# Optimization experiments

Hardware: AMD Instinct MI355X
Metric: run time of the kernel (lower is better)

## Reference

```python
import jax, jax.numpy as jnp
import numpy as np

EMBED_DIM = 1024
NUM_HEADS = 16
HEAD_DIM = EMBED_DIM // NUM_HEADS


def setup_inputs() -> dict:
    key = jax.random.key(0)
    ks = jax.random.split(key, 9)
    s = 1.0 / np.sqrt(EMBED_DIM)
    x = jax.random.normal(ks[0], (2, 2048, EMBED_DIM), dtype=jnp.float32)
    Wq = jax.random.uniform(ks[1], (EMBED_DIM, EMBED_DIM), jnp.float32, -s, s)
    bq = jax.random.uniform(ks[2], (EMBED_DIM,), jnp.float32, -s, s)
    Wk = jax.random.uniform(ks[3], (EMBED_DIM, EMBED_DIM), jnp.float32, -s, s)
    bk = jax.random.uniform(ks[4], (EMBED_DIM,), jnp.float32, -s, s)
    Wv = jax.random.uniform(ks[5], (EMBED_DIM, EMBED_DIM), jnp.float32, -s, s)
    bv = jax.random.uniform(ks[6], (EMBED_DIM,), jnp.float32, -s, s)
    Wo = jax.random.uniform(ks[7], (EMBED_DIM, EMBED_DIM), jnp.float32, -s, s)
    bo = jax.random.uniform(ks[8], (EMBED_DIM,), jnp.float32, -s, s)
    return {"x": x, "Wq": Wq, "bq": bq, "Wk": Wk, "bk": bk,
            "Wv": Wv, "bv": bv, "Wo": Wo, "bo": bo}


def reference(x, Wq, bq, Wk, bk, Wv, bv, Wo, bo):
    B, N, C = x.shape
    H, D = NUM_HEADS, HEAD_DIM
    # nn.Linear: y = x @ W.T + b; here W stored as [in, out] so y = x @ W + b
    def split_heads(y):
        return y.reshape(B, N, H, D).transpose(0, 2, 1, 3)  # [B,H,N,D]
    q = split_heads(x @ Wq + bq)
    k = split_heads(x @ Wk + bk)
    v = split_heads(x @ Wv + bv)
    scores = jnp.einsum('bhnd,bhmd->bhnm', q, k) / jnp.sqrt(jnp.float32(D)).astype(x.dtype)
    attn = jax.nn.softmax(scores, axis=-1)
    ctx = jnp.einsum('bhnm,bhmd->bhnd', attn, v)
    ctx = ctx.transpose(0, 2, 1, 3).reshape(B, N, C)
    return ctx @ Wo + bo
```

## Files before the change

### kernel.cpp

```cpp
#include <hip/hip_runtime.h>
#include <hip/hip_bf16.h>
#include <stdint.h>
#include <stddef.h>

using bf16 = __hip_bfloat16;
using bf16x8 = __attribute__((ext_vector_type(8))) short;
using f32x4  = __attribute__((ext_vector_type(4))) float;
using f32x16 = __attribute__((ext_vector_type(16))) float;
typedef unsigned int u32x2 __attribute__((ext_vector_type(2)));
typedef unsigned int u32x4 __attribute__((ext_vector_type(4)));

#define MFMA16(a, b, c) __builtin_amdgcn_mfma_f32_16x16x32_bf16((a), (b), (c), 0, 0, 0)
#define MFMA32(a, b, c) __builtin_amdgcn_mfma_f32_32x32x16_bf16((a), (b), (c), 0, 0, 0)

#define GLD16(g, l)                                                            \
  __builtin_amdgcn_global_load_lds(                                            \
      (const __attribute__((address_space(1))) void*)(g),                      \
      (__attribute__((address_space(3))) void*)(l), 16, 0, 0)

__device__ __forceinline__ float exp2_fast(float x) {
#if __has_builtin(__builtin_amdgcn_exp2f)
  return __builtin_amdgcn_exp2f(x);
#else
  return __expf(x * 0.69314718056f);
#endif
}

__device__ __forceinline__ unsigned int cvtpk_bf16(float lo, float hi) {
  unsigned int r;
  asm("v_cvt_pk_bf16_f32 %0, %1, %2" : "=v"(r) : "v"(lo), "v"(hi));
  return r;
}

__device__ __forceinline__ void permswap(unsigned int& a, unsigned int& b, int hi) {
#if __has_builtin(__builtin_amdgcn_permlane32_swap)
  u32x2 r = __builtin_amdgcn_permlane32_swap(a, b, false, false);
  a = r.x;
  b = r.y;
#else
  unsigned int sa = __shfl_xor((unsigned int)a, 32, 64);
  unsigned int sb = __shfl_xor((unsigned int)b, 32, 64);
  unsigned int an = hi ? sb : a;
  unsigned int bn = hi ? b : sa;
  a = an; b = bn;
#endif
}


__global__ void convert_x(const float* __restrict__ x, bf16* __restrict__ out) {
  const int i = blockIdx.x * 256 + threadIdx.x;
  const float4 v = ((const float4*)x)[i];
  __hip_bfloat162* o2 = (__hip_bfloat162*)(out + (size_t)i * 4);
  o2[0] = __float22bfloat162_rn(make_float2(v.x, v.y));
  o2[1] = __float22bfloat162_rn(make_float2(v.z, v.w));
}

__global__ void convert_w(const float* __restrict__ W0, const float* __restrict__ W1,
                          const float* __restrict__ W2, const float* __restrict__ W3,
                          bf16* __restrict__ Wt) {
  __shared__ float t[32][33];
  const int bx = blockIdx.x;
  const int mat = bx >> 10;
  const float* W = (mat == 0) ? W0 : (mat == 1) ? W1 : (mat == 2) ? W2 : W3;
  const int rem = bx & 1023;
  const int k0 = (rem >> 5) * 32, n0 = (rem & 31) * 32;
  const int c = threadIdx.x & 31, r0 = (threadIdx.x >> 5) * 4;
#pragma unroll
  for (int i = 0; i < 4; ++i) {
    const int r = r0 + i;
    t[r][c] = W[(size_t)(k0 + r) * 1024 + n0 + c];
  }
  __syncthreads();
  bf16* dst = Wt + (size_t)mat * 1024 * 1024;
#pragma unroll
  for (int i = 0; i < 4; ++i) {
    const int rn = r0 + i;
    dst[(size_t)(n0 + rn) * 1024 + k0 + c] = __float2bfloat16(t[c][rn]);
  }
}

__global__ void concat_bias(const float* __restrict__ bq, const float* __restrict__ bk,
                            const float* __restrict__ bv, const float* __restrict__ bo,
                            float* __restrict__ dst) {
  const int i = blockIdx.x * 256 + threadIdx.x;
  const float* src = (i < 1024) ? bq : (i < 2048) ? bk : (i < 3072) ? bv : bo;
  dst[i] = src[i & 1023];
}


template <int MODE>
__global__ __launch_bounds__(256)
void gemm_bt(const bf16* __restrict__ A, const bf16* __restrict__ Bt,
             const float* __restrict__ bias,
             bf16* __restrict__ Qb, bf16* __restrict__ Kb, bf16* __restrict__ Vt,
             float* __restrict__ Of, int K) {
  __shared__ bf16 As[128 * 32];
  __shared__ bf16 Bs[128 * 32];
  const int tid = threadIdx.x;
  const int lane = tid & 63, w = tid >> 6;
  const int wr = w >> 1, wc = w & 1;
  const int lrow = lane & 15, lgk = lane >> 4;
  const int bm = blockIdx.y * 128, bn = blockIdx.x * 128;
  f32x4 acc[4][4] = {};
  const bf16* Ab = A + (size_t)bm * K;
  const bf16* Bb = Bt + (size_t)bn * K;
  const int e0 = tid, e1 = 256 + tid;

  for (int k0 = 0; k0 < K; k0 += 32) {
    GLD16(Ab + (size_t)(e0 >> 2) * K + k0 + (e0 & 3) * 8, As + e0 * 8);
    GLD16(Ab + (size_t)(e1 >> 2) * K + k0 + (e1 & 3) * 8, As + e1 * 8);
    GLD16(Bb + (size_t)(e0 >> 2) * K + k0 + (e0 & 3) * 8, Bs + e0 * 8);
    GLD16(Bb + (size_t)(e1 >> 2) * K + k0 + (e1 & 3) * 8, Bs + e1 * 8);
    asm volatile("s_waitcnt vmcnt(0)" ::: "memory");
    __syncthreads();
    bf16x8 af[4], bfr[4];
#pragma unroll
    for (int m = 0; m < 4; ++m)
      af[m] = *(const bf16x8*)(As + (wr * 64 + m * 16 + lrow) * 32 + lgk * 8);
#pragma unroll
    for (int n = 0; n < 4; ++n)
      bfr[n] = *(const bf16x8*)(Bs + (wc * 64 + n * 16 + lrow) * 32 + lgk * 8);
#pragma unroll
    for (int m = 0; m < 4; ++m)
#pragma unroll
      for (int n = 0; n < 4; ++n)
        acc[m][n] = MFMA16(af[m], bfr[n], acc[m][n]);
    __syncthreads();
  }

#pragma unroll
  for (int m = 0; m < 4; ++m) {
#pragma unroll
    for (int n = 0; n < 4; ++n) {
      const int col = bn + wc * 64 + n * 16 + lrow;
      const float bv_ = bias[col];
      const int row0 = bm + wr * 64 + m * 16 + lgk * 4;
      if (MODE == 0) {
        const int which = col >> 10;
        const int hd = col & 1023;
        const int h = hd >> 6, d = hd & 63;
#pragma unroll
        for (int j = 0; j < 4; ++j) {
          const int row = row0 + j;
          const int b = row >> 11, t = row & 2047;
          const int bh = b * 16 + h;
          const float v = acc[m][n][j] + bv_;
          if (which == 0)
            Qb[((size_t)bh * 2048 + t) * 64 + d] =
                __float2bfloat16(v * 0.18033688f);
          else if (which == 1)
            Kb[((size_t)bh * 2048 + t) * 64 + d] = __float2bfloat16(v);
          else
            Vt[((size_t)bh * 64 + d) * 2048 + t] = __float2bfloat16(v);
        }
      } else {
#pragma unroll
        for (int j = 0; j < 4; ++j) {
          const int row = row0 + j;
          Of[(size_t)row * 1024 + col] = acc[m][n][j] + bv_;
        }
      }
    }
  }
}

__global__ __launch_bounds__(256)
void attn_kernel(const bf16* __restrict__ Q, const bf16* __restrict__ Kb,
                 const bf16* __restrict__ Vt, bf16* __restrict__ ctx) {
  __shared__ bf16 Kl[2][64 * 64];
  __shared__ bf16 Vl[2][64 * 64];

  const int tid = threadIdx.x, lane = tid & 63, w = tid >> 6;
  const int lo5 = lane & 31, hi = lane >> 5;

  const int bid = blockIdx.x;
  const int xcd = bid & 7, idx = bid >> 3;
  const int bh = (xcd << 2) | (idx >> 4);
  const int qt = idx & 15;
  const int q0 = qt * 128 + w * 32;

  const bf16* Qbh = Q + (size_t)bh * 2048 * 64;
  const bf16* Kbh = Kb + (size_t)bh * 2048 * 64;
  const bf16* Vbh = Vt + (size_t)bh * 64 * 2048;

  bf16x8 qf[4];
#pragma unroll
  for (int f = 0; f < 4; ++f)
    qf[f] = *(const bf16x8*)(Qbh + (size_t)(q0 + lo5) * 64 + f * 16 + hi * 8);

  f32x16 o0 = {}, o1 = {};
  float m2 = -1e30f;
  float lsum = 0.f;

  auto stage = [&](int buf, int kv) {
#pragma unroll
    for (int i = 0; i < 2; ++i) {
      const int c = (w * 2 + i) * 64 + lane;
      const int r = c >> 3, j = c & 7;
      const int js = (j ^ (r & 7)) * 8;
      GLD16(Kbh + (size_t)(kv + r) * 64 + js, &Kl[buf][c * 8]);
      GLD16(Vbh + (size_t)r * 2048 + kv + js, &Vl[buf][c * 8]);
    }
  };

  stage(0, 0);
  asm volatile("s_waitcnt vmcnt(0)" ::: "memory");
  __builtin_amdgcn_s_barrier();
  __builtin_amdgcn_sched_barrier(0);

  for (int t = 0; t < 32; ++t) {
    const int cur = t & 1;
    const int kv = t << 6;
    if (t < 31) {
      stage(cur ^ 1, kv + 64);
      asm volatile("s_waitcnt vmcnt(4)" ::: "memory");
    } else {
      asm volatile("s_waitcnt vmcnt(0)" ::: "memory");
    }
    __builtin_amdgcn_s_barrier();
    __builtin_amdgcn_sched_barrier(0);

    bf16x8 kf[8], vf[8];
#pragma unroll
    for (int kt = 0; kt < 2; ++kt)
#pragma unroll
      for (int f = 0; f < 4; ++f) {
        const int r = kt * 32 + lo5;
        kf[kt * 4 + f] =
            *(const bf16x8*)(&Kl[cur][(r * 8 + (((f << 1) + hi) ^ (r & 7))) * 8]);
      }
#pragma unroll
    for (int dt = 0; dt < 2; ++dt)
#pragma unroll
      for (int ks = 0; ks < 4; ++ks) {
        const int r = dt * 32 + lo5;
        vf[dt * 4 + ks] =
            *(const bf16x8*)(&Vl[cur][(r * 8 + (((ks << 1) + hi) ^ (r & 7))) * 8]);
      }
    asm volatile("s_waitcnt lgkmcnt(0)" ::: "memory");
    __builtin_amdgcn_s_barrier();
    __builtin_amdgcn_sched_barrier(0);

    f32x16 s0 = {}, s1 = {};
#pragma unroll
    for (int f = 0; f < 4; ++f) s0 = MFMA32(kf[f], qf[f], s0);
#pragma unroll
    for (int f = 0; f < 4; ++f) s1 = MFMA32(kf[4 + f], qf[f], s1);

    float p[32];
#pragma unroll
    for (int j = 0; j < 16; ++j) { p[j] = s0[j]; p[16 + j] = s1[j]; }
    float pm = p[0];
#pragma unroll
    for (int j = 1; j < 32; ++j) pm = fmaxf(pm, p[j]);
    if (!__all(pm <= m2 + 11.5416f)) {
      const float mx = fmaxf(pm, __shfl_xor(pm, 32, 64));
      const float mn = fmaxf(m2, mx);
      const float corr = exp2_fast(m2 - mn);
      m2 = mn;
      lsum *= corr;
#pragma unroll
      for (int j = 0; j < 16; ++j) { o0[j] *= corr; o1[j] *= corr; }
    }
    float rs = 0.f;
#pragma unroll
    for (int j = 0; j < 32; ++j) {
      p[j] = exp2_fast(p[j] - m2);
      rs += p[j];
    }
    lsum += rs;

    bf16x8 pa[4];
#pragma unroll
    for (int ks = 0; ks < 4; ++ks) {
      const int b0 = ks * 8;
      unsigned int a0 = cvtpk_bf16(p[b0 + 0], p[b0 + 1]);
      unsigned int c0 = cvtpk_bf16(p[b0 + 4], p[b0 + 5]);
      unsigned int a1 = cvtpk_bf16(p[b0 + 2], p[b0 + 3]);
      unsigned int c1 = cvtpk_bf16(p[b0 + 6], p[b0 + 7]);
      permswap(a0, c0, hi);
      permswap(a1, c1, hi);
      u32x4 tt;
      tt.x = a0; tt.y = a1; tt.z = c0; tt.w = c1;
      pa[ks] = __builtin_bit_cast(bf16x8, tt);
    }

#pragma unroll
    for (int ks = 0; ks < 4; ++ks) {
      o0 = MFMA32(vf[ks], pa[ks], o0);
      o1 = MFMA32(vf[4 + ks], pa[ks], o1);
    }
  }

  lsum += __shfl_xor(lsum, 32, 64);
  const float inv = 1.f / lsum;
  const int b = bh >> 4, h = bh & 15;
  bf16* crow = ctx + (size_t)(b * 2048 + q0 + lo5) * 1024 + h * 64;
#pragma unroll
  for (int g = 0; g < 4; ++g) {
    uint2 pk0, pk1;
    pk0.x = cvtpk_bf16(o0[4 * g + 0] * inv, o0[4 * g + 1] * inv);
    pk0.y = cvtpk_bf16(o0[4 * g + 2] * inv, o0[4 * g + 3] * inv);
    pk1.x = cvtpk_bf16(o1[4 * g + 0] * inv, o1[4 * g + 1] * inv);
    pk1.y = cvtpk_bf16(o1[4 * g + 2] * inv, o1[4 * g + 3] * inv);
    *(uint2*)(crow + 8 * g + 4 * hi) = pk0;
    *(uint2*)(crow + 32 + 8 * g + 4 * hi) = pk1;
  }
}


extern "C" void kernel_launch(void* const* d_in, const int* in_sizes, int n_in,
                              void* d_out, int out_size, void* d_ws, size_t ws_size,
                              hipStream_t stream) {
  const float* x  = (const float*)d_in[0];
  const float* Wq = (const float*)d_in[1];
  const float* bq = (const float*)d_in[2];
  const float* Wk = (const float*)d_in[3];
  const float* bk = (const float*)d_in[4];
  const float* Wv = (const float*)d_in[5];
  const float* bv = (const float*)d_in[6];
  const float* Wo = (const float*)d_in[7];
  const float* bo = (const float*)d_in[8];
  float* out = (float*)d_out;

  char* ws = (char*)d_ws;
  bf16* xb  = (bf16*)(ws);
  bf16* Wt  = (bf16*)(ws + ((size_t)8 << 20));
  bf16* Qb  = (bf16*)(ws + ((size_t)16 << 20));
  bf16* Kb  = (bf16*)(ws + ((size_t)24 << 20));
  bf16* Vt  = (bf16*)(ws + ((size_t)32 << 20));
  bf16* ctx = (bf16*)(ws + ((size_t)40 << 20));
  float* ba = (float*)(ws + ((size_t)48 << 20));

  convert_x<<<dim3(4096), dim3(256), 0, stream>>>(x, xb);
  convert_w<<<dim3(4096), dim3(256), 0, stream>>>(Wq, Wk, Wv, Wo, Wt);
  concat_bias<<<dim3(16), dim3(256), 0, stream>>>(bq, bk, bv, bo, ba);

  gemm_bt<0><<<dim3(24, 32), dim3(256), 0, stream>>>(xb, Wt, ba, Qb, Kb, Vt, nullptr, 1024);

  attn_kernel<<<dim3(512), dim3(256), 0, stream>>>(Qb, Kb, Vt, ctx);

  gemm_bt<1><<<dim3(8, 32), dim3(256), 0, stream>>>(
      ctx, Wt + (size_t)3072 * 1024, ba + 3072, nullptr, nullptr, nullptr, out, 1024);
}
```

Before: 144.2 us.

## Software-pipeline attention softmax with next QK MFMA and stage V-transpose writes

```diff
diff --git a/kernel.cpp b/kernel.cpp
--- a/kernel.cpp
+++ b/kernel.cpp
@@ -24,6 +24,10 @@
 #else
   return __expf(x * 0.69314718056f);
 #endif
+}
+
+__device__ __forceinline__ float fmax3(float a, float b, float c) {
+  return fmaxf(fmaxf(a, b), c);
 }
 
 __device__ __forceinline__ unsigned int cvtpk_bf16(float lo, float hi) {
@@ -128,43 +132,80 @@
     __syncthreads();
   }
 
-#pragma unroll
-  for (int m = 0; m < 4; ++m) {
-#pragma unroll
-    for (int n = 0; n < 4; ++n) {
-      const int col = bn + wc * 64 + n * 16 + lrow;
-      const float bv_ = bias[col];
-      const int row0 = bm + wr * 64 + m * 16 + lgk * 4;
-      if (MODE == 0) {
-        const int which = col >> 10;
-        const int hd = col & 1023;
-        const int h = hd >> 6, d = hd & 63;
-#pragma unroll
-        for (int j = 0; j < 4; ++j) {
-          const int row = row0 + j;
-          const int b = row >> 11, t = row & 2047;
-          const int bh = b * 16 + h;
-          const float v = acc[m][n][j] + bv_;
-          if (which == 0)
-            Qb[((size_t)bh * 2048 + t) * 64 + d] =
-                __float2bfloat16(v * 0.18033688f);
-          else if (which == 1)
-            Kb[((size_t)bh * 2048 + t) * 64 + d] = __float2bfloat16(v);
-          else
-            Vt[((size_t)bh * 64 + d) * 2048 + t] = __float2bfloat16(v);
+  if constexpr (MODE == 0) {
+    if (bn >= 2048) {
+      __shared__ bf16 vstage[64][130];
+      const int b = bm >> 11;
+      const int t0 = bm & 2047;
+      const int h0 = (bn - 2048) >> 6;
+#pragma unroll
+      for (int h2 = 0; h2 < 2; ++h2) {
+        if (wr == h2) {
+#pragma unroll
+          for (int m = 0; m < 4; ++m)
+#pragma unroll
+            for (int n = 0; n < 4; ++n) {
+              const int cl = wc * 64 + n * 16 + lrow;
+              const float bv_ = bias[bn + cl];
+#pragma unroll
+              for (int j = 0; j < 4; ++j)
+                vstage[m * 16 + lgk * 4 + j][cl] =
+                    __float2bfloat16(acc[m][n][j] + bv_);
+            }
         }
-      } else {
-#pragma unroll
-        for (int j = 0; j < 4; ++j) {
-          const int row = row0 + j;
-          Of[(size_t)row * 1024 + col] = acc[m][n][j] + bv_;
+        __syncthreads();
+#pragma unroll
+        for (int it = 0; it < 32; ++it) {
+          const int c = it * 4 + w;
+          const int hh = h0 + (c >> 6), d = c & 63;
+          Vt[((size_t)(b * 16 + hh) * 64 + d) * 2048 + t0 + h2 * 64 + lane] =
+              vstage[lane][c];
         }
-      }
-    }
-  }
-}
-
-__global__ __launch_bounds__(256)
+        __syncthreads();
+      }
+    } else {
+#pragma unroll
+      for (int m = 0; m < 4; ++m) {
+#pragma unroll
+        for (int n = 0; n < 4; ++n) {
+          const int col = bn + wc * 64 + n * 16 + lrow;
+          const float bv_ = bias[col];
+          const int row0 = bm + wr * 64 + m * 16 + lgk * 4;
+          const int which = col >> 10;
+          const int hd = col & 1023;
+          const int h = hd >> 6, d = hd & 63;
+#pragma unroll
+          for (int j = 0; j < 4; ++j) {
+            const int row = row0 + j;
+            const int b = row >> 11, t = row & 2047;
+            const int bh = b * 16 + h;
+            const float v = acc[m][n][j] + bv_;
+            if (which == 0)
+              Qb[((size_t)bh * 2048 + t) * 64 + d] =
+                  __float2bfloat16(v * 0.18033688f);
+            else
+              Kb[((size_t)bh * 2048 + t) * 64 + d] = __float2bfloat16(v);
+          }
+        }
+      }
+    }
+  } else {
+#pragma unroll
+    for (int m = 0; m < 4; ++m) {
+#pragma unroll
+      for (int n = 0; n < 4; ++n) {
+        const int col = bn + wc * 64 + n * 16 + lrow;
+        const float bv_ = bias[col];
+        const int row0 = bm + wr * 64 + m * 16 + lgk * 4;
+#pragma unroll
+        for (int j = 0; j < 4; ++j)
+          Of[(size_t)(row0 + j) * 1024 + col] = acc[m][n][j] + bv_;
+      }
+    }
+  }
+}
+
+__global__ __launch_bounds__(256, 2)
 void attn_kernel(const bf16* __restrict__ Q, const bf16* __restrict__ Kb,
                  const bf16* __restrict__ Vt, bf16* __restrict__ ctx) {
   __shared__ bf16 Kl[2][64 * 64];
@@ -203,56 +244,23 @@
     }
   };
 
-  stage(0, 0);
-  asm volatile("s_waitcnt vmcnt(0)" ::: "memory");
-  __builtin_amdgcn_s_barrier();
-  __builtin_amdgcn_sched_barrier(0);
-
-  for (int t = 0; t < 32; ++t) {
-    const int cur = t & 1;
-    const int kv = t << 6;
-    if (t < 31) {
-      stage(cur ^ 1, kv + 64);
-      asm volatile("s_waitcnt vmcnt(4)" ::: "memory");
-    } else {
-      asm volatile("s_waitcnt vmcnt(0)" ::: "memory");
-    }
-    __builtin_amdgcn_s_barrier();
-    __builtin_amdgcn_sched_barrier(0);
-
-    bf16x8 kf[8], vf[8];
-#pragma unroll
-    for (int kt = 0; kt < 2; ++kt)
-#pragma unroll
-      for (int f = 0; f < 4; ++f) {
-        const int r = kt * 32 + lo5;
-        kf[kt * 4 + f] =
-            *(const bf16x8*)(&Kl[cur][(r * 8 + (((f << 1) + hi) ^ (r & 7))) * 8]);
-      }
-#pragma unroll
-    for (int dt = 0; dt < 2; ++dt)
-#pragma unroll
-      for (int ks = 0; ks < 4; ++ks) {
-        const int r = dt * 32 + lo5;
-        vf[dt * 4 + ks] =
-            *(const bf16x8*)(&Vl[cur][(r * 8 + (((ks << 1) + hi) ^ (r & 7))) * 8]);
-      }
-    asm volatile("s_waitcnt lgkmcnt(0)" ::: "memory");
-    __builtin_amdgcn_s_barrier();
-    __builtin_amdgcn_sched_barrier(0);
-
-    f32x16 s0 = {}, s1 = {};
-#pragma unroll
-    for (int f = 0; f < 4; ++f) s0 = MFMA32(kf[f], qf[f], s0);
-#pragma unroll
-    for (int f = 0; f < 4; ++f) s1 = MFMA32(kf[4 + f], qf[f], s1);
-
-    float p[32];
-#pragma unroll
-    for (int j = 0; j < 16; ++j) { p[j] = s0[j]; p[16 + j] = s1[j]; }
-    float pm = p[0];
-#pragma unroll
-    for (int j = 1; j < 32; ++j) pm = fmaxf(pm, p[j]);
+  bf16x8 pa[4];
+
+  auto softmax_pa = [&](f32x16& s0, f32x16& s1) {
+    float r1[11];
+#pragma unroll
+    for (int i = 0; i < 5; ++i)
+      r1[i] = fmax3(s0[3 * i], s0[3 * i + 1], s0[3 * i + 2]);
+    r1[5] = fmax3(s0[15], s1[0], s1[1]);
+#pragma unroll
+    for (int i = 0; i < 4; ++i)
+      r1[6 + i] = fmax3(s1[2 + 3 * i], s1[3 + 3 * i], s1[4 + 3 * i]);
+    r1[10] = fmaxf(s1[14], s1[15]);
+    float r2[4];
+#pragma unroll
+    for (int i = 0; i < 3; ++i) r2[i] = fmax3(r1[3 * i], r1[3 * i + 1], r1[3 * i + 2]);
+    r2[3] = fmaxf(r1[9], r1[10]);
+    const float pm = fmaxf(fmax3(r2[0], r2[1], r2[2]), r2[3]);
     if (!__all(pm <= m2 + 11.5416f)) {
       const float mx = fmaxf(pm, __shfl_xor(pm, 32, 64));
       const float mn = fmaxf(m2, mx);
@@ -262,34 +270,98 @@
 #pragma unroll
       for (int j = 0; j < 16; ++j) { o0[j] *= corr; o1[j] *= corr; }
     }
-    float rs = 0.f;
-#pragma unroll
-    for (int j = 0; j < 32; ++j) {
-      p[j] = exp2_fast(p[j] - m2);
-      rs += p[j];
-    }
-    lsum += rs;
-
-    bf16x8 pa[4];
+#pragma unroll
+    for (int j = 0; j < 16; ++j) s0[j] = exp2_fast(s0[j] - m2);
+#pragma unroll
+    for (int j = 0; j < 16; ++j) s1[j] = exp2_fast(s1[j] - m2);
+    float a8[8];
+#pragma unroll
+    for (int j = 0; j < 8; ++j) a8[j] = (s0[j] + s0[j + 8]) + (s1[j] + s1[j + 8]);
+    float a4[4];
+#pragma unroll
+    for (int j = 0; j < 4; ++j) a4[j] = a8[j] + a8[j + 4];
+    lsum += (a4[0] + a4[1]) + (a4[2] + a4[3]);
 #pragma unroll
     for (int ks = 0; ks < 4; ++ks) {
-      const int b0 = ks * 8;
-      unsigned int a0 = cvtpk_bf16(p[b0 + 0], p[b0 + 1]);
-      unsigned int c0 = cvtpk_bf16(p[b0 + 4], p[b0 + 5]);
-      unsigned int a1 = cvtpk_bf16(p[b0 + 2], p[b0 + 3]);
-      unsigned int c1 = cvtpk_bf16(p[b0 + 6], p[b0 + 7]);
+      const f32x16& s = (ks < 2) ? s0 : s1;
+      const int b0 = (ks & 1) * 8;
+      unsigned int a0 = cvtpk_bf16(s[b0 + 0], s[b0 + 1]);
+      unsigned int c0 = cvtpk_bf16(s[b0 + 4], s[b0 + 5]);
+      unsigned int a1 = cvtpk_bf16(s[b0 + 2], s[b0 + 3]);
+      unsigned int c1 = cvtpk_bf16(s[b0 + 6], s[b0 + 7]);
       permswap(a0, c0, hi);
       permswap(a1, c1, hi);
       u32x4 tt;
       tt.x = a0; tt.y = a1; tt.z = c0; tt.w = c1;
       pa[ks] = __builtin_bit_cast(bf16x8, tt);
     }
-
-#pragma unroll
-    for (int ks = 0; ks < 4; ++ks) {
-      o0 = MFMA32(vf[ks], pa[ks], o0);
-      o1 = MFMA32(vf[4 + ks], pa[ks], o1);
-    }
+  };
+
+  f32x16 sA0, sA1, sB0, sB1;
+  bf16x8 vfA[8], vfB[8];
+
+  auto step = [&](int t, f32x16& sC0, f32x16& sC1, bf16x8 (&vfC)[8],
+                  f32x16& sP0, f32x16& sP1, bf16x8 (&vfP)[8]) {
+    const int cur = t & 1;
+    const int kv = t << 6;
+    if (t < 31) stage(cur ^ 1, kv + 64);
+    if (t < 31)
+      asm volatile("s_waitcnt vmcnt(4)" ::: "memory");
+    else
+      asm volatile("s_waitcnt vmcnt(0)" ::: "memory");
+    __builtin_amdgcn_s_barrier();
+    bf16x8 kf[8];
+#pragma unroll
+    for (int kt = 0; kt < 2; ++kt)
+#pragma unroll
+      for (int f = 0; f < 4; ++f) {
+        const int r = kt * 32 + lo5;
+        kf[kt * 4 + f] =
+            *(const bf16x8*)(&Kl[cur][(r * 8 + (((f << 1) + hi) ^ (r & 7))) * 8]);
+      }
+#pragma unroll
+    for (int dt = 0; dt < 2; ++dt)
+#pragma unroll
+      for (int ks = 0; ks < 4; ++ks) {
+        const int r = dt * 32 + lo5;
+        vfC[dt * 4 + ks] =
+            *(const bf16x8*)(&Vl[cur][(r * 8 + (((ks << 1) + hi) ^ (r & 7))) * 8]);
+      }
+    if (t > 0) softmax_pa(sP0, sP1);
+    asm volatile("s_waitcnt lgkmcnt(0)" ::: "memory");
+    __builtin_amdgcn_sched_barrier(0);
+    __builtin_amdgcn_s_barrier();
+    __builtin_amdgcn_s_setprio(1);
+    sC0 = f32x16{};
+    sC1 = f32x16{};
+#pragma unroll
+    for (int f = 0; f < 4; ++f) sC0 = MFMA32(kf[f], qf[f], sC0);
+#pragma unroll
+    for (int f = 0; f < 4; ++f) sC1 = MFMA32(kf[4 + f], qf[f], sC1);
+    if (t > 0) {
+#pragma unroll
+      for (int ks = 0; ks < 4; ++ks) {
+        o0 = MFMA32(vfP[ks], pa[ks], o0);
+        o1 = MFMA32(vfP[4 + ks], pa[ks], o1);
+      }
+    }
+    __builtin_amdgcn_s_setprio(0);
+  };
+
+  stage(0, 0);
+
+  step(0, sA0, sA1, vfA, sB0, sB1, vfB);
+  for (int tt = 1; tt < 31; tt += 2) {
+    step(tt, sB0, sB1, vfB, sA0, sA1, vfA);
+    step(tt + 1, sA0, sA1, vfA, sB0, sB1, vfB);
+  }
+  step(31, sB0, sB1, vfB, sA0, sA1, vfA);
+
+  softmax_pa(sB0, sB1);
+#pragma unroll
+  for (int ks = 0; ks < 4; ++ks) {
+    o0 = MFMA32(vfB[ks], pa[ks], o0);
+    o1 = MFMA32(vfB[4 + ks], pa[ks], o1);
   }
 
   lsum += __shfl_xor(lsum, 32, 64);
```

Result: no change. 145.8 us (+1.1%).
